# Kernel optimization log

Measured on AMD Instinct MI355X. Metric: run time of the kernel, lower is better.

The kernel has to match this reference:

```python
import jax, jax.numpy as jnp
import numpy as np


def make_hadamard(n, seed=1):
    # Sylvester Hadamard matrix with random sign diagonal, orthonormalized.
    assert (n & (n - 1)) == 0, 'n must be a power of 2'
    H = np.array([[1.0]], dtype=np.float32)
    while H.shape[0] < n:
        H = np.block([[H, H], [H, -H]])
    rng = np.random.default_rng(seed)
    signs = rng.choice(np.array([-1.0, 1.0], dtype=np.float32), size=n)
    H = (H * signs[None, :]) / np.sqrt(n, dtype=np.float32)
    return jnp.asarray(H)


def setup_inputs() -> dict:
    key = jax.random.key(0)
    k_x, = jax.random.split(key, 1)
    B, S, D = 4, 4096, 2048
    x = jax.random.normal(k_x, (B, S, D), dtype=jnp.float32)
    scale = jnp.ones((1,), dtype=jnp.float32) * 0.1  # must be > 0
    hadamard = make_hadamard(D)
    return {
        'x': x,
        'scale': scale,
        'hadamard': hadamard,
        'Qn': 8,
        'Qp': 7,
        'num_elements': B * S * D,
    }


def reference(x, scale, hadamard, Qn, Qp, num_elements):
    # grad_scale_mode == 'LSQ_grad_scale'
    qn = float(Qn)
    qp = float(Qp)
    grad_scale = 1.0 / jnp.sqrt(jnp.float32(num_elements) * qp)
    # scale = (scale - scale*gs).detach() + scale*gs  (forward value unchanged)
    bw_scale = scale * grad_scale
    s = jax.lax.stop_gradient(scale - bw_scale) + bw_scale  # shape [1]

    x_rot = jnp.matmul(x, hadamard)           # [B,S,D]
    xq = jnp.clip(x_rot / s, -qn, qp)
    # straight-through rounding: (round(x)-x).detach() + x
    yq = jax.lax.stop_gradient(jnp.round(xq) - xq) + xq
    y = yq * s
    return jnp.matmul(y, hadamard.T)          # un-rotate
```

## Files before the change

### kernel.cpp

```cpp
#include <hip/hip_runtime.h>
#include <math.h>


constexpr int D  = 2048;
constexpr int NR = 8;

#define LGKM0() __asm__ __volatile__("s_waitcnt lgkmcnt(0)" ::: "memory")

typedef unsigned uint2v __attribute__((ext_vector_type(2)));
typedef float    f4v    __attribute__((ext_vector_type(4)));

__device__ __forceinline__ void bfly(float4& a, float4& b) {
    float4 ta = a, tb = b;
    a.x = ta.x + tb.x; a.y = ta.y + tb.y; a.z = ta.z + tb.z; a.w = ta.w + tb.w;
    b.x = ta.x - tb.x; b.y = ta.y - tb.y; b.z = ta.z - tb.z; b.w = ta.w - tb.w;
}

__device__ __forceinline__ void reg_stages(float4 (&v)[NR]) {
    #pragma unroll
    for (int m = 1; m <= 4; m <<= 1) {
        #pragma unroll
        for (int r = 0; r < NR; ++r)
            if ((r & m) == 0) bfly(v[r], v[r | m]);
    }
}

__device__ __forceinline__ void comp_stages(float4 (&v)[NR]) {
    #pragma unroll
    for (int r = 0; r < NR; ++r) {
        float a, b;
        a = v[r].x; b = v[r].y; v[r].x = a + b; v[r].y = a - b;
        a = v[r].z; b = v[r].w; v[r].z = a + b; v[r].w = a - b;
        a = v[r].x; b = v[r].z; v[r].x = a + b; v[r].z = a - b;
        a = v[r].y; b = v[r].w; v[r].y = a + b; v[r].w = a - b;
    }
}

__device__ __forceinline__ void plswap32(float& x, float& y) {
#if __has_builtin(__builtin_amdgcn_permlane32_swap)
    uint2v t = __builtin_amdgcn_permlane32_swap(
        __builtin_bit_cast(unsigned, x), __builtin_bit_cast(unsigned, y),
        false, false);
    x = __builtin_bit_cast(float, t[0]);
    y = __builtin_bit_cast(float, t[1]);
#else
    asm volatile("v_permlane32_swap_b32 %0, %1" : "+v"(x), "+v"(y));
#endif
}
__device__ __forceinline__ void plswap16(float& x, float& y) {
#if __has_builtin(__builtin_amdgcn_permlane16_swap)
    uint2v t = __builtin_amdgcn_permlane16_swap(
        __builtin_bit_cast(unsigned, x), __builtin_bit_cast(unsigned, y),
        false, false);
    x = __builtin_bit_cast(float, t[0]);
    y = __builtin_bit_cast(float, t[1]);
#else
    asm volatile("v_permlane16_swap_b32 %0, %1" : "+v"(x), "+v"(y));
#endif
}

template<bool IS32>
__device__ __forceinline__ int probe_var(int lane) {
    const int m = IS32 ? 32 : 16;
    float a = (float)lane, b = 1000.0f + (float)lane;
    if (IS32) plswap32(a, b); else plswap16(a, b);
    const bool hi = (lane & m) != 0;
    const float ea0 = hi ? 1000.0f + (float)(lane - m) : (float)lane;
    const float eb0 = hi ? 1000.0f + (float)lane       : (float)(lane + m);
    const float ea2 = hi ? (float)lane                 : 1000.0f + (float)(lane + m);
    const float eb2 = hi ? (float)(lane - m)           : 1000.0f + (float)lane;
    if (__all(a == ea0 && b == eb0)) return 0;
    if (__all(a == eb0 && b == ea0)) return 1;
    if (__all(a == ea2 && b == eb2)) return 2;
    if (__all(a == eb2 && b == ea2)) return 3;
    return 4;
}

template<int VAR, bool IS32>
__device__ __forceinline__ void bfly_l(float& a, float& b) {
    if (IS32) plswap32(a, b); else plswap16(a, b);
    float s = a + b;
    float d = (VAR == 0 || VAR == 3) ? (a - b) : (b - a);
    if (VAR == 0)      { if (IS32) plswap32(s, d); else plswap16(s, d); a = s; b = d; }
    else if (VAR == 1) { if (IS32) plswap32(s, d); else plswap16(s, d); a = d; b = s; }
    else if (VAR == 2) { if (IS32) plswap32(d, s); else plswap16(d, s); a = d; b = s; }
    else               { if (IS32) plswap32(d, s); else plswap16(d, s); a = s; b = d; }
}

__device__ __forceinline__ void shfl_stage(float4 (&v)[NR], int m, int lane) {
    const bool hi = (lane & m) != 0;
    #pragma unroll
    for (int r = 0; r < NR; ++r) {
        float t;
        t = __shfl_xor(v[r].x, m); v[r].x = hi ? t - v[r].x : v[r].x + t;
        t = __shfl_xor(v[r].y, m); v[r].y = hi ? t - v[r].y : v[r].y + t;
        t = __shfl_xor(v[r].z, m); v[r].z = hi ? t - v[r].z : v[r].z + t;
        t = __shfl_xor(v[r].w, m); v[r].w = hi ? t - v[r].w : v[r].w + t;
    }
}

template<int VAR, bool IS32>
__device__ __forceinline__ void perm_stage(float4 (&v)[NR], int lane) {
    if constexpr (VAR == 4) {
        shfl_stage(v, IS32 ? 32 : 16, lane);
    } else {
        #pragma unroll
        for (int r = 0; r < NR; r += 2) {
            bfly_l<VAR, IS32>(v[r].x, v[r + 1].x);
            bfly_l<VAR, IS32>(v[r].y, v[r + 1].y);
            bfly_l<VAR, IS32>(v[r].z, v[r + 1].z);
            bfly_l<VAR, IS32>(v[r].w, v[r + 1].w);
        }
    }
}

__device__ __forceinline__ float quant1(float xh, float h0, float s, float inv_s,
                                        float nqn, float qp) {
    float u = xh * h0 * inv_s;
    u = fminf(fmaxf(u, nqn), qp);
    float q = rintf(u);
    return q * (s * h0);
}

template<int VAR>
__device__ __forceinline__ void fwht_body(
    const float* __restrict__ x, const float* __restrict__ hadamard,
    float* __restrict__ out, float* lds, int lane, int row,
    float s, float inv_s, float nqn, float qp)
{
    float4 v[NR];
    {
        const float4* x4 = reinterpret_cast<const float4*>(x + (size_t)row * D) + lane;
        #pragma unroll
        for (int r = 0; r < NR; ++r) v[r] = x4[(size_t)r * 64];
    }

    const int rB0 = (((lane >> 5) & 1) << 5) + ((lane & 31) << 6);

    float4 h[NR];
    {
        const float* hp = hadamard + rB0;
        #pragma unroll
        for (int q = 0; q < NR; ++q)
            h[q] = *reinterpret_cast<const float4*>(hp + (q << 2));
    }

    const int wA0 = (lane << 2) ^ (((lane >> 4) & 3) << 2);
    const int l7s = (lane & 7) << 2;

    comp_stages(v);
    reg_stages(v);
    perm_stage<VAR, false>(v, lane);
    perm_stage<VAR, true >(v, lane);
    #pragma unroll
    for (int r = 0; r < NR; ++r)
        *reinterpret_cast<float4*>(lds + (r << 8) + (wA0 ^ ((r & 1) << 4))) = v[r];
    LGKM0();
    #pragma unroll
    for (int q = 0; q < NR; ++q)
        v[q] = *reinterpret_cast<const float4*>(lds + rB0 + ((q << 2) ^ l7s));
    reg_stages(v);
    perm_stage<VAR, true >(v, lane);

    #pragma unroll
    for (int r = 0; r < NR; ++r) {
        v[r].x = quant1(v[r].x, h[r].x, s, inv_s, nqn, qp);
        v[r].y = quant1(v[r].y, h[r].y, s, inv_s, nqn, qp);
        v[r].z = quant1(v[r].z, h[r].z, s, inv_s, nqn, qp);
        v[r].w = quant1(v[r].w, h[r].w, s, inv_s, nqn, qp);
    }

    reg_stages(v);
    perm_stage<VAR, true >(v, lane);
    #pragma unroll
    for (int q = 0; q < NR; ++q)
        *reinterpret_cast<float4*>(lds + rB0 + ((q << 2) ^ l7s)) = v[q];
    LGKM0();
    #pragma unroll
    for (int r = 0; r < NR; ++r)
        v[r] = *reinterpret_cast<const float4*>(lds + (r << 8) + (wA0 ^ ((r & 1) << 4)));
    reg_stages(v);
    perm_stage<VAR, false>(v, lane);
    perm_stage<VAR, true >(v, lane);
    comp_stages(v);

    {
        f4v* y4 = reinterpret_cast<f4v*>(out + (size_t)row * D) + lane;
        #pragma unroll
        for (int r = 0; r < NR; ++r)
            __builtin_nontemporal_store(__builtin_bit_cast(f4v, v[r]),
                                        &y4[(size_t)r * 64]);
    }
}

__global__ __launch_bounds__(256) void lsq_fwht_kernel(
    const float* __restrict__ x,
    const float* __restrict__ scale,
    const float* __restrict__ hadamard,
    const int*   __restrict__ qn_p,
    const int*   __restrict__ qp_p,
    const int*   __restrict__ ne_p,
    float*       __restrict__ out,
    int rows)
{
    __shared__ float smem[4][D];

    const int lane = threadIdx.x & 63;
    const int wave = threadIdx.x >> 6;
    const int row  = blockIdx.x * 4 + wave;
    if (row >= rows) return;

    float* lds = smem[wave];

    const int p32 = probe_var<true>(lane);
    const int p16 = probe_var<false>(lane);
    const int var = (p32 == p16) ? p32 : 4;

    const float sc    = scale[0];
    const float qp    = (float)qp_p[0];
    const float nqn   = -(float)qn_p[0];
    const float gs    = 1.0f / sqrtf((float)ne_p[0] * qp);
    const float bw    = sc * gs;
    const float s     = (sc - bw) + bw;
    const float inv_s = 1.0f / s;

    switch (var) {
    case 0:  fwht_body<0>(x, hadamard, out, lds, lane, row, s, inv_s, nqn, qp); break;
    case 1:  fwht_body<1>(x, hadamard, out, lds, lane, row, s, inv_s, nqn, qp); break;
    case 2:  fwht_body<2>(x, hadamard, out, lds, lane, row, s, inv_s, nqn, qp); break;
    case 3:  fwht_body<3>(x, hadamard, out, lds, lane, row, s, inv_s, nqn, qp); break;
    default: fwht_body<4>(x, hadamard, out, lds, lane, row, s, inv_s, nqn, qp); break;
    }
}

extern "C" void kernel_launch(void* const* d_in, const int* in_sizes, int n_in,
                              void* d_out, int out_size, void* d_ws, size_t ws_size,
                              hipStream_t stream) {
    const float* x        = (const float*)d_in[0];
    const float* scale    = (const float*)d_in[1];
    const float* hadamard = (const float*)d_in[2];
    const int*   Qn       = (const int*)d_in[3];
    const int*   Qp       = (const int*)d_in[4];
    const int*   ne       = (const int*)d_in[5];
    float*       out      = (float*)d_out;

    const int rows = in_sizes[0] / D;
    const int grid = (rows + 3) / 4;

    lsq_fwht_kernel<<<grid, 256, 0, stream>>>(x, scale, hadamard, Qn, Qp, ne,
                                              out, rows);
}
```

Before: 251.7 us.

## Process two rows per wave and interleave their FWHT stages to overlap LDS traffic

Each wave now handles two rows, loading both up front and interleaving the butterfly, permutation, LDS exchange and quantization phases of row A and row B so one row's LDS round-trip waits overlap the other row's ALU work. The grid is halved to match. The Hadamard sign vector is loaded once and shared by both rows. This roughly doubles the register footprint per thread, which may reduce occupancy, and leaves fewer workgroups to spread across the GPU.

```diff
diff --git a/kernel.cpp b/kernel.cpp
--- a/kernel.cpp
+++ b/kernel.cpp
@@ -122,46 +122,8 @@
     return q * (s * h0);
 }
 
-template<int VAR>
-__device__ __forceinline__ void fwht_body(
-    const float* __restrict__ x, const float* __restrict__ hadamard,
-    float* __restrict__ out, float* lds, int lane, int row,
-    float s, float inv_s, float nqn, float qp)
-{
-    float4 v[NR];
-    {
-        const float4* x4 = reinterpret_cast<const float4*>(x + (size_t)row * D) + lane;
-        #pragma unroll
-        for (int r = 0; r < NR; ++r) v[r] = x4[(size_t)r * 64];
-    }
-
-    const int rB0 = (((lane >> 5) & 1) << 5) + ((lane & 31) << 6);
-
-    float4 h[NR];
-    {
-        const float* hp = hadamard + rB0;
-        #pragma unroll
-        for (int q = 0; q < NR; ++q)
-            h[q] = *reinterpret_cast<const float4*>(hp + (q << 2));
-    }
-
-    const int wA0 = (lane << 2) ^ (((lane >> 4) & 3) << 2);
-    const int l7s = (lane & 7) << 2;
-
-    comp_stages(v);
-    reg_stages(v);
-    perm_stage<VAR, false>(v, lane);
-    perm_stage<VAR, true >(v, lane);
-    #pragma unroll
-    for (int r = 0; r < NR; ++r)
-        *reinterpret_cast<float4*>(lds + (r << 8) + (wA0 ^ ((r & 1) << 4))) = v[r];
-    LGKM0();
-    #pragma unroll
-    for (int q = 0; q < NR; ++q)
-        v[q] = *reinterpret_cast<const float4*>(lds + rB0 + ((q << 2) ^ l7s));
-    reg_stages(v);
-    perm_stage<VAR, true >(v, lane);
-
+__device__ __forceinline__ void quant_all(float4 (&v)[NR], const float4 (&h)[NR],
+                                          float s, float inv_s, float nqn, float qp) {
     #pragma unroll
     for (int r = 0; r < NR; ++r) {
         v[r].x = quant1(v[r].x, h[r].x, s, inv_s, nqn, qp);
@@ -169,26 +131,115 @@
         v[r].z = quant1(v[r].z, h[r].z, s, inv_s, nqn, qp);
         v[r].w = quant1(v[r].w, h[r].w, s, inv_s, nqn, qp);
     }
-
+}
+
+template<int VAR>
+__device__ __forceinline__ void p1a(float4 (&v)[NR]) {
+    comp_stages(v); reg_stages(v);
+}
+template<int VAR>
+__device__ __forceinline__ void p1b(float4 (&v)[NR], int lane) {
+    perm_stage<VAR, false>(v, lane); perm_stage<VAR, true>(v, lane);
+}
+template<int VAR>
+__device__ __forceinline__ void p2(float4 (&v)[NR], int lane) {
+    reg_stages(v); perm_stage<VAR, true>(v, lane);
+}
+template<int VAR>
+__device__ __forceinline__ void p4(float4 (&v)[NR], int lane) {
     reg_stages(v);
-    perm_stage<VAR, true >(v, lane);
+    perm_stage<VAR, false>(v, lane); perm_stage<VAR, true>(v, lane);
+    comp_stages(v);
+}
+
+__device__ __forceinline__ void wAB(float* lds, const float4 (&v)[NR], int wA0) {
+    #pragma unroll
+    for (int r = 0; r < NR; ++r)
+        *reinterpret_cast<float4*>(lds + (r << 8) + (wA0 ^ ((r & 1) << 4))) = v[r];
+}
+__device__ __forceinline__ void rAB(float* lds, float4 (&v)[NR], int rB0, int l7s) {
+    #pragma unroll
+    for (int q = 0; q < NR; ++q)
+        v[q] = *reinterpret_cast<const float4*>(lds + rB0 + ((q << 2) ^ l7s));
+}
+__device__ __forceinline__ void wBA(float* lds, const float4 (&v)[NR], int rB0, int l7s) {
     #pragma unroll
     for (int q = 0; q < NR; ++q)
         *reinterpret_cast<float4*>(lds + rB0 + ((q << 2) ^ l7s)) = v[q];
-    LGKM0();
+}
+__device__ __forceinline__ void rBA(float* lds, float4 (&v)[NR], int wA0) {
     #pragma unroll
     for (int r = 0; r < NR; ++r)
         v[r] = *reinterpret_cast<const float4*>(lds + (r << 8) + (wA0 ^ ((r & 1) << 4)));
-    reg_stages(v);
-    perm_stage<VAR, false>(v, lane);
-    perm_stage<VAR, true >(v, lane);
-    comp_stages(v);
-
+}
+
+template<int VAR>
+__device__ __forceinline__ void fwht_body(
+    const float* __restrict__ x, const float* __restrict__ hadamard,
+    float* __restrict__ out, float* lds, int lane, int rowA, int rowB, bool doB,
+    float s, float inv_s, float nqn, float qp)
+{
+    float4 vA[NR], vB[NR], h[NR];
     {
-        f4v* y4 = reinterpret_cast<f4v*>(out + (size_t)row * D) + lane;
+        const float4* xa4 = reinterpret_cast<const float4*>(x + (size_t)rowA * D) + lane;
+        const float4* xb4 = reinterpret_cast<const float4*>(x + (size_t)rowB * D) + lane;
+        #pragma unroll
+        for (int r = 0; r < NR; ++r) vA[r] = xa4[(size_t)r * 64];
+        #pragma unroll
+        for (int r = 0; r < NR; ++r) vB[r] = xb4[(size_t)r * 64];
+    }
+
+    const int rB0 = (((lane >> 5) & 1) << 5) + ((lane & 31) << 6);
+    const int wA0 = (lane << 2) ^ (((lane >> 4) & 3) << 2);
+    const int l7s = (lane & 7) << 2;
+
+    float4* hv = (float4*)h;
+    {
+        const float* hp = hadamard + rB0;
+        #pragma unroll
+        for (int q = 0; q < NR; ++q)
+            hv[q] = *reinterpret_cast<const float4*>(hp + (q << 2));
+    }
+
+    p1a<VAR>(vA); p1b<VAR>(vA, lane);
+    wAB(lds, vA, wA0);
+    p1a<VAR>(vB);
+    LGKM0();
+    rAB(lds, vA, rB0, l7s);
+    p1b<VAR>(vB, lane);
+    LGKM0();
+    wAB(lds, vB, wA0);
+    p2<VAR>(vA, lane);
+    quant_all(vA, h, s, inv_s, nqn, qp);
+    LGKM0();
+    rAB(lds, vB, rB0, l7s);
+    p2<VAR>(vA, lane);
+    LGKM0();
+    wBA(lds, vA, rB0, l7s);
+    p2<VAR>(vB, lane);
+    quant_all(vB, h, s, inv_s, nqn, qp);
+    LGKM0();
+    rBA(lds, vA, wA0);
+    p2<VAR>(vB, lane);
+    LGKM0();
+    wBA(lds, vB, rB0, l7s);
+    p4<VAR>(vA, lane);
+    LGKM0();
+    rBA(lds, vB, wA0);
+    {
+        f4v* y4 = reinterpret_cast<f4v*>(out + (size_t)rowA * D) + lane;
         #pragma unroll
         for (int r = 0; r < NR; ++r)
-            __builtin_nontemporal_store(__builtin_bit_cast(f4v, v[r]),
+            __builtin_nontemporal_store(__builtin_bit_cast(f4v, vA[r]),
+                                        &y4[(size_t)r * 64]);
+    }
+    LGKM0();
+    p4<VAR>(vB, lane);
+    if (doB) {
+        f4v* y4 = reinterpret_cast<f4v*>(out + (size_t)rowB * D) + lane;
+        #pragma unroll
+        for (int r = 0; r < NR; ++r)
+            __builtin_nontemporal_store(__builtin_bit_cast(f4v, vB[r]),
                                         &y4[(size_t)r * 64]);
     }
 }
@@ -207,14 +258,16 @@
 
     const int lane = threadIdx.x & 63;
     const int wave = threadIdx.x >> 6;
-    const int row  = blockIdx.x * 4 + wave;
-    if (row >= rows) return;
+    const int rowA = blockIdx.x * 8 + wave * 2;
+    if (rowA >= rows) return;
+    const bool doB = (rowA + 1) < rows;
+    const int rowB = doB ? rowA + 1 : rowA;
 
     float* lds = smem[wave];
 
-    const int p32 = probe_var<true>(lane);
-    const int p16 = probe_var<false>(lane);
-    const int var = (p32 == p16) ? p32 : 4;
+    const int p32v = probe_var<true>(lane);
+    const int p16v = probe_var<false>(lane);
+    const int var  = (p32v == p16v) ? p32v : 4;
 
     const float sc    = scale[0];
     const float qp    = (float)qp_p[0];
@@ -225,11 +278,11 @@
     const float inv_s = 1.0f / s;
 
     switch (var) {
-    case 0:  fwht_body<0>(x, hadamard, out, lds, lane, row, s, inv_s, nqn, qp); break;
-    case 1:  fwht_body<1>(x, hadamard, out, lds, lane, row, s, inv_s, nqn, qp); break;
-    case 2:  fwht_body<2>(x, hadamard, out, lds, lane, row, s, inv_s, nqn, qp); break;
-    case 3:  fwht_body<3>(x, hadamard, out, lds, lane, row, s, inv_s, nqn, qp); break;
-    default: fwht_body<4>(x, hadamard, out, lds, lane, row, s, inv_s, nqn, qp); break;
+    case 0:  fwht_body<0>(x, hadamard, out, lds, lane, rowA, rowB, doB, s, inv_s, nqn, qp); break;
+    case 1:  fwht_body<1>(x, hadamard, out, lds, lane, rowA, rowB, doB, s, inv_s, nqn, qp); break;
+    case 2:  fwht_body<2>(x, hadamard, out, lds, lane, rowA, rowB, doB, s, inv_s, nqn, qp); break;
+    case 3:  fwht_body<3>(x, hadamard, out, lds, lane, rowA, rowB, doB, s, inv_s, nqn, qp); break;
+    default: fwht_body<4>(x, hadamard, out, lds, lane, rowA, rowB, doB, s, inv_s, nqn, qp); break;
     }
 }
 
@@ -245,7 +298,7 @@
     float*       out      = (float*)d_out;
 
     const int rows = in_sizes[0] / D;
-    const int grid = (rows + 3) / 4;
+    const int grid = (rows + 7) / 8;
 
     lsq_fwht_kernel<<<grid, 256, 0, stream>>>(x, scale, hadamard, Qn, Qp, ne,
                                               out, rows);
```

After: 260.0 us. 1.03x slower.

## Make kernel persistent with grid-stride rows and prefetch next row into registers

Applied to the files above, without the earlier changes.

Caps the grid at 1024 blocks and has each wave loop over rows with a stride of the total wave count. While the current row goes through the butterfly, LDS and quantize stages, the next row's input is loaded into a second register buffer, hiding global load latency. The hadamard sign loads and setup are amortized across rows. Doubling the row registers raises VGPR pressure and may lower occupancy.

```diff
diff --git a/kernel.cpp b/kernel.cpp
--- a/kernel.cpp
+++ b/kernel.cpp
@@ -122,46 +122,8 @@
     return q * (s * h0);
 }
 
-template<int VAR>
-__device__ __forceinline__ void fwht_body(
-    const float* __restrict__ x, const float* __restrict__ hadamard,
-    float* __restrict__ out, float* lds, int lane, int row,
-    float s, float inv_s, float nqn, float qp)
-{
-    float4 v[NR];
-    {
-        const float4* x4 = reinterpret_cast<const float4*>(x + (size_t)row * D) + lane;
-        #pragma unroll
-        for (int r = 0; r < NR; ++r) v[r] = x4[(size_t)r * 64];
-    }
-
-    const int rB0 = (((lane >> 5) & 1) << 5) + ((lane & 31) << 6);
-
-    float4 h[NR];
-    {
-        const float* hp = hadamard + rB0;
-        #pragma unroll
-        for (int q = 0; q < NR; ++q)
-            h[q] = *reinterpret_cast<const float4*>(hp + (q << 2));
-    }
-
-    const int wA0 = (lane << 2) ^ (((lane >> 4) & 3) << 2);
-    const int l7s = (lane & 7) << 2;
-
-    comp_stages(v);
-    reg_stages(v);
-    perm_stage<VAR, false>(v, lane);
-    perm_stage<VAR, true >(v, lane);
-    #pragma unroll
-    for (int r = 0; r < NR; ++r)
-        *reinterpret_cast<float4*>(lds + (r << 8) + (wA0 ^ ((r & 1) << 4))) = v[r];
-    LGKM0();
-    #pragma unroll
-    for (int q = 0; q < NR; ++q)
-        v[q] = *reinterpret_cast<const float4*>(lds + rB0 + ((q << 2) ^ l7s));
-    reg_stages(v);
-    perm_stage<VAR, true >(v, lane);
-
+__device__ __forceinline__ void quant_all(float4 (&v)[NR], const float4 (&h)[NR],
+                                          float s, float inv_s, float nqn, float qp) {
     #pragma unroll
     for (int r = 0; r < NR; ++r) {
         v[r].x = quant1(v[r].x, h[r].x, s, inv_s, nqn, qp);
@@ -169,27 +131,108 @@
         v[r].z = quant1(v[r].z, h[r].z, s, inv_s, nqn, qp);
         v[r].w = quant1(v[r].w, h[r].w, s, inv_s, nqn, qp);
     }
-
-    reg_stages(v);
-    perm_stage<VAR, true >(v, lane);
+}
+
+__device__ __forceinline__ void wAB(float* lds, const float4 (&v)[NR], int wA0) {
+    #pragma unroll
+    for (int r = 0; r < NR; ++r)
+        *reinterpret_cast<float4*>(lds + (r << 8) + (wA0 ^ ((r & 1) << 4))) = v[r];
+}
+__device__ __forceinline__ void rAB(float* lds, float4 (&v)[NR], int rB0, int l7s) {
+    #pragma unroll
+    for (int q = 0; q < NR; ++q)
+        v[q] = *reinterpret_cast<const float4*>(lds + rB0 + ((q << 2) ^ l7s));
+}
+__device__ __forceinline__ void wBA(float* lds, const float4 (&v)[NR], int rB0, int l7s) {
     #pragma unroll
     for (int q = 0; q < NR; ++q)
         *reinterpret_cast<float4*>(lds + rB0 + ((q << 2) ^ l7s)) = v[q];
-    LGKM0();
+}
+__device__ __forceinline__ void rBA(float* lds, float4 (&v)[NR], int wA0) {
     #pragma unroll
     for (int r = 0; r < NR; ++r)
         v[r] = *reinterpret_cast<const float4*>(lds + (r << 8) + (wA0 ^ ((r & 1) << 4)));
+}
+
+template<int VAR>
+__device__ __forceinline__ void row_step(
+    const float* __restrict__ x, float* __restrict__ out,
+    float* lds, int lane, int row, int nrow, int rows,
+    float4 (&v)[NR], float4 (&vN)[NR], const float4 (&h)[NR],
+    int rB0, int wA0, int l7s,
+    float s, float inv_s, float nqn, float qp)
+{
+    if (nrow < rows) {
+        const float4* x4 = reinterpret_cast<const float4*>(x + (size_t)nrow * D) + lane;
+        #pragma unroll
+        for (int r = 0; r < NR; ++r) vN[r] = x4[(size_t)r * 64];
+    }
+
+    comp_stages(v);
     reg_stages(v);
     perm_stage<VAR, false>(v, lane);
     perm_stage<VAR, true >(v, lane);
+    wAB(lds, v, wA0);
+    LGKM0();
+    rAB(lds, v, rB0, l7s);
+    reg_stages(v);
+    perm_stage<VAR, true >(v, lane);
+
+    quant_all(v, h, s, inv_s, nqn, qp);
+
+    reg_stages(v);
+    perm_stage<VAR, true >(v, lane);
+    wBA(lds, v, rB0, l7s);
+    LGKM0();
+    rBA(lds, v, wA0);
+    reg_stages(v);
+    perm_stage<VAR, false>(v, lane);
+    perm_stage<VAR, true >(v, lane);
     comp_stages(v);
 
+    f4v* y4 = reinterpret_cast<f4v*>(out + (size_t)row * D) + lane;
+    #pragma unroll
+    for (int r = 0; r < NR; ++r)
+        __builtin_nontemporal_store(__builtin_bit_cast(f4v, v[r]),
+                                    &y4[(size_t)r * 64]);
+}
+
+template<int VAR>
+__device__ __forceinline__ void fwht_body(
+    const float* __restrict__ x, const float* __restrict__ hadamard,
+    float* __restrict__ out, float* lds, int lane, int gwave, int nwaves,
+    int rows, float s, float inv_s, float nqn, float qp)
+{
+    const int rB0 = (((lane >> 5) & 1) << 5) + ((lane & 31) << 6);
+    const int wA0 = (lane << 2) ^ (((lane >> 4) & 3) << 2);
+    const int l7s = (lane & 7) << 2;
+
+    float4 h[NR];
     {
-        f4v* y4 = reinterpret_cast<f4v*>(out + (size_t)row * D) + lane;
-        #pragma unroll
-        for (int r = 0; r < NR; ++r)
-            __builtin_nontemporal_store(__builtin_bit_cast(f4v, v[r]),
-                                        &y4[(size_t)r * 64]);
+        const float* hp = hadamard + rB0;
+        #pragma unroll
+        for (int q = 0; q < NR; ++q)
+            h[q] = *reinterpret_cast<const float4*>(hp + (q << 2));
+    }
+
+    float4 vA[NR], vB[NR];
+    int row = gwave;
+    {
+        const float4* x4 = reinterpret_cast<const float4*>(x + (size_t)row * D) + lane;
+        #pragma unroll
+        for (int r = 0; r < NR; ++r) vA[r] = x4[(size_t)r * 64];
+    }
+
+    for (;;) {
+        int nrow = row + nwaves;
+        row_step<VAR>(x, out, lds, lane, row, nrow, rows, vA, vB, h,
+                      rB0, wA0, l7s, s, inv_s, nqn, qp);
+        if (nrow >= rows) break;
+        row = nrow; nrow = row + nwaves;
+        row_step<VAR>(x, out, lds, lane, row, nrow, rows, vB, vA, h,
+                      rB0, wA0, l7s, s, inv_s, nqn, qp);
+        if (nrow >= rows) break;
+        row = nrow;
     }
 }
 
@@ -205,16 +248,17 @@
 {
     __shared__ float smem[4][D];
 
-    const int lane = threadIdx.x & 63;
-    const int wave = threadIdx.x >> 6;
-    const int row  = blockIdx.x * 4 + wave;
-    if (row >= rows) return;
+    const int lane   = threadIdx.x & 63;
+    const int wave   = threadIdx.x >> 6;
+    const int gwave  = blockIdx.x * 4 + wave;
+    const int nwaves = gridDim.x * 4;
+    if (gwave >= rows) return;
 
     float* lds = smem[wave];
 
-    const int p32 = probe_var<true>(lane);
-    const int p16 = probe_var<false>(lane);
-    const int var = (p32 == p16) ? p32 : 4;
+    const int p32v = probe_var<true>(lane);
+    const int p16v = probe_var<false>(lane);
+    const int var  = (p32v == p16v) ? p32v : 4;
 
     const float sc    = scale[0];
     const float qp    = (float)qp_p[0];
@@ -225,11 +269,11 @@
     const float inv_s = 1.0f / s;
 
     switch (var) {
-    case 0:  fwht_body<0>(x, hadamard, out, lds, lane, row, s, inv_s, nqn, qp); break;
-    case 1:  fwht_body<1>(x, hadamard, out, lds, lane, row, s, inv_s, nqn, qp); break;
-    case 2:  fwht_body<2>(x, hadamard, out, lds, lane, row, s, inv_s, nqn, qp); break;
-    case 3:  fwht_body<3>(x, hadamard, out, lds, lane, row, s, inv_s, nqn, qp); break;
-    default: fwht_body<4>(x, hadamard, out, lds, lane, row, s, inv_s, nqn, qp); break;
+    case 0:  fwht_body<0>(x, hadamard, out, lds, lane, gwave, nwaves, rows, s, inv_s, nqn, qp); break;
+    case 1:  fwht_body<1>(x, hadamard, out, lds, lane, gwave, nwaves, rows, s, inv_s, nqn, qp); break;
+    case 2:  fwht_body<2>(x, hadamard, out, lds, lane, gwave, nwaves, rows, s, inv_s, nqn, qp); break;
+    case 3:  fwht_body<3>(x, hadamard, out, lds, lane, gwave, nwaves, rows, s, inv_s, nqn, qp); break;
+    default: fwht_body<4>(x, hadamard, out, lds, lane, gwave, nwaves, rows, s, inv_s, nqn, qp); break;
     }
 }
 
@@ -245,7 +289,8 @@
     float*       out      = (float*)d_out;
 
     const int rows = in_sizes[0] / D;
-    const int grid = (rows + 3) / 4;
+    int grid = (rows + 3) / 4;
+    if (grid > 1024) grid = 1024;
 
     lsq_fwht_kernel<<<grid, 256, 0, stream>>>(x, scale, hadamard, Qn, Qp, ne,
                                               out, rows);
```

Result: no change. 254.2 us (+1.0%).

## Replace LDS transpose with in-register DPP/swizzle butterflies for FWHT

Applied to the files above, without the earlier changes.

Removes the LDS-based transpose between butterfly stages. The transform now runs with element-in-register stages plus cross-lane stages using DPP quad permutes, ds_swizzle and permlane swaps, so each row is handled entirely in registers by one wave. This drops the shared memory allocation, and launch bounds now request a minimum occupancy. The trade-off is more cross-lane instructions per stage (six lane stages per transform instead of mixing in LDS), plus an extra runtime probe.

```diff
diff --git a/kernel.cpp b/kernel.cpp
--- a/kernel.cpp
+++ b/kernel.cpp
@@ -4,8 +4,6 @@
 
 constexpr int D  = 2048;
 constexpr int NR = 8;
-
-#define LGKM0() __asm__ __volatile__("s_waitcnt lgkmcnt(0)" ::: "memory")
 
 typedef unsigned uint2v __attribute__((ext_vector_type(2)));
 typedef float    f4v    __attribute__((ext_vector_type(4)));
@@ -33,6 +31,55 @@
         a = v[r].z; b = v[r].w; v[r].z = a + b; v[r].w = a - b;
         a = v[r].x; b = v[r].z; v[r].x = a + b; v[r].z = a - b;
         a = v[r].y; b = v[r].w; v[r].y = a + b; v[r].w = a - b;
+    }
+}
+
+template<int CTRL>
+__device__ __forceinline__ float dpp_partner(float x) {
+#if __has_builtin(__builtin_amdgcn_update_dpp)
+    return __builtin_bit_cast(float, __builtin_amdgcn_update_dpp(
+        0, __builtin_bit_cast(int, x), CTRL, 0xF, 0xF, true));
+#else
+    return 0.0f;
+#endif
+}
+
+template<int OFF>
+__device__ __forceinline__ float dsz_partner(float x) {
+#if __has_builtin(__builtin_amdgcn_ds_swizzle)
+    return __builtin_bit_cast(float, __builtin_amdgcn_ds_swizzle(
+        __builtin_bit_cast(int, x), OFF));
+#else
+    return 0.0f;
+#endif
+}
+
+template<int CTRL>
+__device__ __forceinline__ void dpp_stage(float4 (&v)[NR], float sgn) {
+    #pragma unroll
+    for (int r = 0; r < NR; ++r) {
+        float tx = dpp_partner<CTRL>(v[r].x);
+        float ty = dpp_partner<CTRL>(v[r].y);
+        float tz = dpp_partner<CTRL>(v[r].z);
+        float tw = dpp_partner<CTRL>(v[r].w);
+        v[r].x = fmaf(sgn, v[r].x, tx);
+        v[r].y = fmaf(sgn, v[r].y, ty);
+        v[r].z = fmaf(sgn, v[r].z, tz);
+        v[r].w = fmaf(sgn, v[r].w, tw);
+    }
+}
+template<int OFF>
+__device__ __forceinline__ void dsz_stage(float4 (&v)[NR], float sgn) {
+    #pragma unroll
+    for (int r = 0; r < NR; ++r) {
+        float tx = dsz_partner<OFF>(v[r].x);
+        float ty = dsz_partner<OFF>(v[r].y);
+        float tz = dsz_partner<OFF>(v[r].z);
+        float tw = dsz_partner<OFF>(v[r].w);
+        v[r].x = fmaf(sgn, v[r].x, tx);
+        v[r].y = fmaf(sgn, v[r].y, ty);
+        v[r].z = fmaf(sgn, v[r].z, tz);
+        v[r].w = fmaf(sgn, v[r].w, tw);
     }
 }
 
@@ -76,6 +123,16 @@
     return 4;
 }
 
+__device__ __forceinline__ bool probe_fast(int lane) {
+    float a = (float)lane;
+    bool ok = true;
+    ok = ok && __all(dpp_partner<0xB1>(a)   == (float)(lane ^ 1));
+    ok = ok && __all(dpp_partner<0x4E>(a)   == (float)(lane ^ 2));
+    ok = ok && __all(dsz_partner<0x101F>(a) == (float)(lane ^ 4));
+    ok = ok && __all(dsz_partner<0x201F>(a) == (float)(lane ^ 8));
+    return ok;
+}
+
 template<int VAR, bool IS32>
 __device__ __forceinline__ void bfly_l(float& a, float& b) {
     if (IS32) plswap32(a, b); else plswap16(a, b);
@@ -87,6 +144,17 @@
     else               { if (IS32) plswap32(d, s); else plswap16(d, s); a = s; b = d; }
 }
 
+template<int VAR, bool IS32>
+__device__ __forceinline__ void perm_stage(float4 (&v)[NR]) {
+    #pragma unroll
+    for (int r = 0; r < NR; r += 2) {
+        bfly_l<VAR, IS32>(v[r].x, v[r + 1].x);
+        bfly_l<VAR, IS32>(v[r].y, v[r + 1].y);
+        bfly_l<VAR, IS32>(v[r].z, v[r + 1].z);
+        bfly_l<VAR, IS32>(v[r].w, v[r + 1].w);
+    }
+}
+
 __device__ __forceinline__ void shfl_stage(float4 (&v)[NR], int m, int lane) {
     const bool hi = (lane & m) != 0;
     #pragma unroll
@@ -99,18 +167,22 @@
     }
 }
 
-template<int VAR, bool IS32>
-__device__ __forceinline__ void perm_stage(float4 (&v)[NR], int lane) {
-    if constexpr (VAR == 4) {
-        shfl_stage(v, IS32 ? 32 : 16, lane);
+template<int VAR>
+__device__ __forceinline__ void fwht_full(float4 (&v)[NR], int lane,
+                                          float s1, float s2, float s4, float s8) {
+    comp_stages(v);
+    reg_stages(v);
+    if constexpr (VAR < 4) {
+        dpp_stage<0xB1>(v, s1);
+        dpp_stage<0x4E>(v, s2);
+        dsz_stage<0x101F>(v, s4);
+        dsz_stage<0x201F>(v, s8);
+        perm_stage<VAR, false>(v);
+        perm_stage<VAR, true >(v);
     } else {
-        #pragma unroll
-        for (int r = 0; r < NR; r += 2) {
-            bfly_l<VAR, IS32>(v[r].x, v[r + 1].x);
-            bfly_l<VAR, IS32>(v[r].y, v[r + 1].y);
-            bfly_l<VAR, IS32>(v[r].z, v[r + 1].z);
-            bfly_l<VAR, IS32>(v[r].w, v[r + 1].w);
-        }
+        shfl_stage(v, 1, lane);  shfl_stage(v, 2, lane);
+        shfl_stage(v, 4, lane);  shfl_stage(v, 8, lane);
+        shfl_stage(v, 16, lane); shfl_stage(v, 32, lane);
     }
 }
 
@@ -125,42 +197,25 @@
 template<int VAR>
 __device__ __forceinline__ void fwht_body(
     const float* __restrict__ x, const float* __restrict__ hadamard,
-    float* __restrict__ out, float* lds, int lane, int row,
+    float* __restrict__ out, int lane, int row,
     float s, float inv_s, float nqn, float qp)
 {
-    float4 v[NR];
+    const float s1 = (lane & 1) ? -1.0f : 1.0f;
+    const float s2 = (lane & 2) ? -1.0f : 1.0f;
+    const float s4 = (lane & 4) ? -1.0f : 1.0f;
+    const float s8 = (lane & 8) ? -1.0f : 1.0f;
+
+    float4 v[NR], h[NR];
     {
         const float4* x4 = reinterpret_cast<const float4*>(x + (size_t)row * D) + lane;
+        const float4* h4 = reinterpret_cast<const float4*>(hadamard) + lane;
         #pragma unroll
         for (int r = 0; r < NR; ++r) v[r] = x4[(size_t)r * 64];
-    }
-
-    const int rB0 = (((lane >> 5) & 1) << 5) + ((lane & 31) << 6);
-
-    float4 h[NR];
-    {
-        const float* hp = hadamard + rB0;
         #pragma unroll
-        for (int q = 0; q < NR; ++q)
-            h[q] = *reinterpret_cast<const float4*>(hp + (q << 2));
-    }
-
-    const int wA0 = (lane << 2) ^ (((lane >> 4) & 3) << 2);
-    const int l7s = (lane & 7) << 2;
-
-    comp_stages(v);
-    reg_stages(v);
-    perm_stage<VAR, false>(v, lane);
-    perm_stage<VAR, true >(v, lane);
-    #pragma unroll
-    for (int r = 0; r < NR; ++r)
-        *reinterpret_cast<float4*>(lds + (r << 8) + (wA0 ^ ((r & 1) << 4))) = v[r];
-    LGKM0();
-    #pragma unroll
-    for (int q = 0; q < NR; ++q)
-        v[q] = *reinterpret_cast<const float4*>(lds + rB0 + ((q << 2) ^ l7s));
-    reg_stages(v);
-    perm_stage<VAR, true >(v, lane);
+        for (int r = 0; r < NR; ++r) h[r] = h4[(size_t)r * 64];
+    }
+
+    fwht_full<VAR>(v, lane, s1, s2, s4, s8);
 
     #pragma unroll
     for (int r = 0; r < NR; ++r) {
@@ -170,30 +225,16 @@
         v[r].w = quant1(v[r].w, h[r].w, s, inv_s, nqn, qp);
     }
 
-    reg_stages(v);
-    perm_stage<VAR, true >(v, lane);
-    #pragma unroll
-    for (int q = 0; q < NR; ++q)
-        *reinterpret_cast<float4*>(lds + rB0 + ((q << 2) ^ l7s)) = v[q];
-    LGKM0();
+    fwht_full<VAR>(v, lane, s1, s2, s4, s8);
+
+    f4v* y4 = reinterpret_cast<f4v*>(out + (size_t)row * D) + lane;
     #pragma unroll
     for (int r = 0; r < NR; ++r)
-        v[r] = *reinterpret_cast<const float4*>(lds + (r << 8) + (wA0 ^ ((r & 1) << 4)));
-    reg_stages(v);
-    perm_stage<VAR, false>(v, lane);
-    perm_stage<VAR, true >(v, lane);
-    comp_stages(v);
-
-    {
-        f4v* y4 = reinterpret_cast<f4v*>(out + (size_t)row * D) + lane;
-        #pragma unroll
-        for (int r = 0; r < NR; ++r)
-            __builtin_nontemporal_store(__builtin_bit_cast(f4v, v[r]),
-                                        &y4[(size_t)r * 64]);
-    }
-}
-
-__global__ __launch_bounds__(256) void lsq_fwht_kernel(
+        __builtin_nontemporal_store(__builtin_bit_cast(f4v, v[r]),
+                                    &y4[(size_t)r * 64]);
+}
+
+__global__ __launch_bounds__(256, 4) void lsq_fwht_kernel(
     const float* __restrict__ x,
     const float* __restrict__ scale,
     const float* __restrict__ hadamard,
@@ -203,18 +244,14 @@
     float*       __restrict__ out,
     int rows)
 {
-    __shared__ float smem[4][D];
-
     const int lane = threadIdx.x & 63;
     const int wave = threadIdx.x >> 6;
     const int row  = blockIdx.x * 4 + wave;
     if (row >= rows) return;
 
-    float* lds = smem[wave];
-
-    const int p32 = probe_var<true>(lane);
-    const int p16 = probe_var<false>(lane);
-    const int var = (p32 == p16) ? p32 : 4;
+    const int p32v = probe_var<true>(lane);
+    const int p16v = probe_var<false>(lane);
+    const int var  = (p32v == p16v && probe_fast(lane)) ? p32v : 4;
 
     const float sc    = scale[0];
     const float qp    = (float)qp_p[0];
@@ -225,11 +262,11 @@
     const float inv_s = 1.0f / s;
 
     switch (var) {
-    case 0:  fwht_body<0>(x, hadamard, out, lds, lane, row, s, inv_s, nqn, qp); break;
-    case 1:  fwht_body<1>(x, hadamard, out, lds, lane, row, s, inv_s, nqn, qp); break;
-    case 2:  fwht_body<2>(x, hadamard, out, lds, lane, row, s, inv_s, nqn, qp); break;
-    case 3:  fwht_body<3>(x, hadamard, out, lds, lane, row, s, inv_s, nqn, qp); break;
-    default: fwht_body<4>(x, hadamard, out, lds, lane, row, s, inv_s, nqn, qp); break;
+    case 0:  fwht_body<0>(x, hadamard, out, lane, row, s, inv_s, nqn, qp); break;
+    case 1:  fwht_body<1>(x, hadamard, out, lane, row, s, inv_s, nqn, qp); break;
+    case 2:  fwht_body<2>(x, hadamard, out, lane, row, s, inv_s, nqn, qp); break;
+    case 3:  fwht_body<3>(x, hadamard, out, lane, row, s, inv_s, nqn, qp); break;
+    default: fwht_body<4>(x, hadamard, out, lane, row, s, inv_s, nqn, qp); break;
     }
 }
 
```

Measured after the change: 260.9 us. 1.04x slower.
